# Kernel optimization log

Measured on AMD Instinct MI355X. Metric: run time of the kernel, lower is better.

## Reference

```python
import jax, jax.numpy as jnp
import numpy as np

VOCAB = 50257
EMBED = 512


def setup_inputs() -> dict:
    key = jax.random.key(0)
    k_idx, k_w = jax.random.split(key)
    input = jax.random.randint(k_idx, (8, 4096), 0, VOCAB, dtype=jnp.int64 if jax.config.jax_enable_x64 else jnp.int32)
    weight = jax.random.normal(k_w, (VOCAB, EMBED), dtype=jnp.float32)
    return {"input": input, "weight": weight}


def reference(input, weight):
    # one_hot(input, V) @ weight  ==  weight[input]  (exact same math,
    # since one-hot matmul just selects rows). Expressed as an indexed
    # gather, the efficient/idiomatic form.
    return jnp.take(weight, input, axis=0)  # [..., E]
```

## Files before the change

kernel.cpp:

```cpp
#include <hip/hip_runtime.h>
#include <hip/hip_bf16.h>


#define EMBED_F4 128
#define N_IDX    (8 * 4096)
#define TOTAL_F4 (N_IDX * EMBED_F4)

__global__ __launch_bounds__(256) void Embedding_60327110640045_kernel(
    const int* __restrict__ idx,
    const float4* __restrict__ weight,
    float4* __restrict__ out)
{
    int tid = blockIdx.x * blockDim.x + threadIdx.x;
    if (tid >= TOTAL_F4) return;
    int row = tid >> 7;
    int col = tid & 127;
    int w_row = idx[row];
    out[tid] = weight[(long long)w_row * EMBED_F4 + col];
}

extern "C" void kernel_launch(void* const* d_in, const int* in_sizes, int n_in,
                              void* d_out, int out_size, void* d_ws, size_t ws_size,
                              hipStream_t stream) {
    const int*    idx    = (const int*)d_in[0];
    const float4* weight = (const float4*)d_in[1];
    float4*       out    = (float4*)d_out;

    const int block = 256;
    const int grid  = (TOTAL_F4 + block - 1) / block;
    Embedding_60327110640045_kernel<<<grid, block, 0, stream>>>(idx, weight, out);
}
```

Baseline: 162.9 us.

## Assign four embedding rows per wavefront with scalar row indices and batched loads

Each 64-lane wavefront now handles four embedding rows: it loads four indices as one int4, makes them wave-uniform with readfirstlane, issues eight independent float4 loads, then writes them out. The aim is to cut per-thread index loads and address arithmetic and to raise memory-level parallelism with more loads in flight per thread. The grid shrinks by a factor of eight, which lowers the number of resident waves and may reduce latency hiding.

After: 163.3 us. No clear change (+0.3%).

```diff
diff --git a/kernel.cpp b/kernel.cpp
--- a/kernel.cpp
+++ b/kernel.cpp
@@ -2,21 +2,49 @@
 #include <hip/hip_bf16.h>
 
 
-#define EMBED_F4 128
-#define N_IDX    (8 * 4096)
-#define TOTAL_F4 (N_IDX * EMBED_F4)
+#define EMBED_F4  128
+#define N_IDX     (8 * 4096)
+#define ROWS_PER_WAVE 4
+#define N_WAVES   (N_IDX / ROWS_PER_WAVE)
 
 __global__ __launch_bounds__(256) void Embedding_60327110640045_kernel(
     const int* __restrict__ idx,
     const float4* __restrict__ weight,
     float4* __restrict__ out)
 {
-    int tid = blockIdx.x * blockDim.x + threadIdx.x;
-    if (tid >= TOTAL_F4) return;
-    int row = tid >> 7;
-    int col = tid & 127;
-    int w_row = idx[row];
-    out[tid] = weight[(long long)w_row * EMBED_F4 + col];
+    const int gtid = blockIdx.x * blockDim.x + threadIdx.x;
+    const int wave = gtid >> 6;
+    const int lane = threadIdx.x & 63;
+
+    const int4 rows4 = ((const int4*)idx)[wave];
+    const int r0 = __builtin_amdgcn_readfirstlane(rows4.x);
+    const int r1 = __builtin_amdgcn_readfirstlane(rows4.y);
+    const int r2 = __builtin_amdgcn_readfirstlane(rows4.z);
+    const int r3 = __builtin_amdgcn_readfirstlane(rows4.w);
+
+    const float4* __restrict__ s0 = weight + (size_t)r0 * EMBED_F4;
+    const float4* __restrict__ s1 = weight + (size_t)r1 * EMBED_F4;
+    const float4* __restrict__ s2 = weight + (size_t)r2 * EMBED_F4;
+    const float4* __restrict__ s3 = weight + (size_t)r3 * EMBED_F4;
+
+    float4 a0 = s0[lane];
+    float4 a1 = s0[lane + 64];
+    float4 b0 = s1[lane];
+    float4 b1 = s1[lane + 64];
+    float4 c0 = s2[lane];
+    float4 c1 = s2[lane + 64];
+    float4 d0 = s3[lane];
+    float4 d1 = s3[lane + 64];
+
+    float4* __restrict__ dst = out + (size_t)wave * (ROWS_PER_WAVE * EMBED_F4);
+    dst[lane]       = a0;
+    dst[lane + 64]  = a1;
+    dst[lane + 128] = b0;
+    dst[lane + 192] = b1;
+    dst[lane + 256] = c0;
+    dst[lane + 320] = c1;
+    dst[lane + 384] = d0;
+    dst[lane + 448] = d1;
 }
 
 extern "C" void kernel_launch(void* const* d_in, const int* in_sizes, int n_in,
@@ -27,6 +55,6 @@
     float4*       out    = (float4*)d_out;
 
     const int block = 256;
-    const int grid  = (TOTAL_F4 + block - 1) / block;
+    const int grid  = N_WAVES * 64 / block;
     Embedding_60327110640045_kernel<<<grid, block, 0, stream>>>(idx, weight, out);
 }
```
